# Kernel optimization log

Hardware: AMD Instinct MI355X
Metric: run time of the kernel (lower is better)

## Reference

```python
import jax, jax.numpy as jnp
import numpy as np

BATCH, L, D_OUT, D_HID = 8, 8192, 512, 256
R_MIN, R_MAX, MAX_PHASE = 0.9, 0.999, 6.28


def setup_inputs() -> dict:
    key = jax.random.key(0)
    ks = jax.random.split(key, 10)
    x = jax.random.normal(ks[0], (BATCH, L, D_OUT), jnp.float32)
    # input_dense (nn.Dense(d_out)) params
    W = jax.random.normal(ks[1], (D_OUT, D_OUT), jnp.float32) / jnp.sqrt(jnp.float32(D_OUT))
    b = jnp.zeros((D_OUT,), jnp.float32)
    # nu_log / theta_log per the flax initializers
    u1 = jax.random.uniform(ks[2], (D_HID,), jnp.float32)
    nu_log = jnp.log(-0.5 * jnp.log(u1 * (R_MAX**2 - R_MIN**2) + R_MIN**2))
    u2 = jax.random.uniform(ks[3], (D_HID,), jnp.float32)
    theta_log = jnp.log(MAX_PHASE * u2)
    diag_lambda = jnp.exp(-jnp.exp(nu_log) + 1j * jnp.exp(theta_log))
    gamma_log = jnp.log(jnp.sqrt(1.0 - jnp.abs(diag_lambda) ** 2))
    B_re = jax.random.normal(ks[4], (D_HID, D_OUT), jnp.float32) / jnp.sqrt(jnp.float32(2 * D_OUT))
    B_im = jax.random.normal(ks[5], (D_HID, D_OUT), jnp.float32) / jnp.sqrt(jnp.float32(2 * D_OUT))
    C_re = jax.random.normal(ks[6], (D_OUT, D_HID), jnp.float32) / jnp.sqrt(jnp.float32(D_HID))
    C_im = jax.random.normal(ks[7], (D_OUT, D_HID), jnp.float32) / jnp.sqrt(jnp.float32(D_HID))
    D = jax.random.normal(ks[8], (D_OUT,), jnp.float32)
    return {"x": x, "W": W, "b": b, "nu_log": nu_log, "theta_log": theta_log,
            "gamma_log": gamma_log, "B_re": B_re, "B_im": B_im,
            "C_re": C_re, "C_im": C_im, "D": D}


def _binop(q_i, q_j):
    # associative op for diagonal linear recurrence h_t = A_t h_{t-1} + b_t
    A_i, b_i = q_i
    A_j, b_j = q_j
    return (A_j * A_i, A_j * b_i + b_j)


def reference(x, W, b, nu_log, theta_log, gamma_log, B_re, B_im, C_re, C_im, D):
    xp = x @ W + b                                            # [B,L,d_out]
    lam = jnp.exp(-jnp.exp(nu_log) + 1j * jnp.exp(theta_log))  # [N] complex
    B_norm = (B_re + 1j * B_im) * jnp.exp(gamma_log)[:, None]  # [N,d_out]
    Bu = xp.astype(B_norm.dtype) @ B_norm.T                    # [B,L,N] complex
    Lam = jnp.broadcast_to(lam, Bu.shape)
    # parallel scan over sequence axis (axis=1); elementwise binop, batch broadcasts
    _, h = jax.lax.associative_scan(_binop, (Lam, Bu), axis=1)  # [B,L,N]
    C = C_re + 1j * C_im                                        # [d_out,N]
    outputs = jnp.real(h @ C.T) + D * xp                        # [B,L,d_out]
    return outputs, h[:, -1]
```

## Files before the change

kernel.cpp:

```cpp
#include <hip/hip_runtime.h>
#include <hip/hip_bf16.h>
#include <math.h>

#define BATCH   8
#define SEQL    8192
#define DOUTD   512
#define DHID    256
#define MTOT    (BATCH*SEQL)
#define CHUNKS  128
#define CHUNKLN 64
#define SQUAR   6

typedef __bf16 bh;
typedef __bf16 bh8 __attribute__((ext_vector_type(8)));
typedef __bf16 bh2 __attribute__((ext_vector_type(2)));
typedef float  f32x4 __attribute__((ext_vector_type(4)));


__global__ void setup_kernel(const float4* __restrict__ x, bh* __restrict__ xh,
                             const float* __restrict__ W, float* __restrict__ Wt,
                             const float* __restrict__ nu_log, const float* __restrict__ theta_log,
                             const float* __restrict__ gamma_log, const float* __restrict__ Bre,
                             const float* __restrict__ Bim, const float* __restrict__ bvec,
                             const float* __restrict__ Dvec,
                             float* lamRe, float* lamIm, float* lamSRe, float* lamSIm,
                             float* gamma, float* bB, float* bD) {
    int bid = blockIdx.x;
    const int tid = threadIdx.x;
    if (bid < 16384) {
        long i = (long)bid * 256 + tid;
        float4 a = x[2 * i], c = x[2 * i + 1];
        bh8 o;
        o[0] = (bh)a.x; o[1] = (bh)a.y; o[2] = (bh)a.z; o[3] = (bh)a.w;
        o[4] = (bh)c.x; o[5] = (bh)c.y; o[6] = (bh)c.z; o[7] = (bh)c.w;
        *(bh8*)(xh + i * 8) = o;
        return;
    }
    bid -= 16384;
    if (bid < 64) {
        __shared__ float t[64][65];
        const int bx = bid & 7, by = bid >> 3;
        const int r0 = by * 64, c0 = bx * 64;
        const int tr = tid >> 4;
        const int tc = (tid & 15) * 4;
#pragma unroll
        for (int rr = 0; rr < 64; rr += 16) {
            float4 v = *(const float4*)&W[(size_t)(r0 + tr + rr) * 512 + c0 + tc];
            t[tr + rr][tc + 0] = v.x; t[tr + rr][tc + 1] = v.y;
            t[tr + rr][tc + 2] = v.z; t[tr + rr][tc + 3] = v.w;
        }
        __syncthreads();
#pragma unroll
        for (int rr = 0; rr < 64; rr += 16) {
            const int orow = tr + rr;
            float4 o;
            o.x = t[tc + 0][orow]; o.y = t[tc + 1][orow];
            o.z = t[tc + 2][orow]; o.w = t[tc + 3][orow];
            *(float4*)&Wt[(size_t)(c0 + orow) * 512 + r0 + tc] = o;
        }
        return;
    }
    bid -= 64;
    if (bid == 0) {
        for (int t = tid; t < 512; t += 256) bD[t] = bvec[t] * Dvec[t];
        int t = tid;
        if (t < 256) {
            float nu = expf(nu_log[t]);
            float th = expf(theta_log[t]);
            float mag = expf(-nu);
            float lr = mag * cosf(th), li = mag * sinf(th);
            lamRe[t] = lr; lamIm[t] = li;
            float pr = lr, pi = li;
            for (int s = 0; s < SQUAR; ++s) { float nr = pr*pr - pi*pi, ni = 2.f*pr*pi; pr = nr; pi = ni; }
            lamSRe[t] = pr; lamSIm[t] = pi;
            gamma[t] = expf(gamma_log[t]);
        }
        return;
    }
    const int t = bid - 1;
    __shared__ float rr[256], ri[256];
    float b0 = bvec[tid], b1 = bvec[tid + 256];
    float pr = b0 * Bre[(size_t)t * 512 + tid] + b1 * Bre[(size_t)t * 512 + tid + 256];
    float pi = b0 * Bim[(size_t)t * 512 + tid] + b1 * Bim[(size_t)t * 512 + tid + 256];
    rr[tid] = pr; ri[tid] = pi;
    __syncthreads();
    for (int s = 128; s > 0; s >>= 1) {
        if (tid < s) { rr[tid] += rr[tid + s]; ri[tid] += ri[tid + s]; }
        __syncthreads();
    }
    if (tid == 0) {
        float g = expf(gamma_log[t]);
        bB[2 * t]     = rr[0] * g;
        bB[2 * t + 1] = ri[0] * g;
    }
}

__global__ void prepBC_kernel(const float* __restrict__ Wt, const float* __restrict__ Bre,
                              const float* __restrict__ Bim, const float* __restrict__ gamma,
                              bh* __restrict__ WBt,
                              const float* __restrict__ Cre, const float* __restrict__ Cim,
                              const float* __restrict__ Dvec, bh* __restrict__ WcT) {
    if (blockIdx.x < 128) {
        __shared__ float bsh[4][512];
        const int c0 = blockIdx.x * 4;
        const int tid = threadIdx.x;
        for (int i = tid; i < 2048; i += 256) {
            int ci = i >> 9, k = i & 511;
            int c = c0 + ci;
            float v = (c < 256) ? Bre[(size_t)c * 512 + k] : Bim[(size_t)(c - 256) * 512 + k];
            bsh[ci][k] = v * gamma[c & 255];
        }
        __syncthreads();
        const int j = tid * 2;
        float a0[4] = {}, a1[4] = {};
        for (int k = 0; k < 512; ++k) {
            float2 wv = *(const float2*)&Wt[(size_t)k * 512 + j];
#pragma unroll
            for (int ci = 0; ci < 4; ++ci) {
                float b = bsh[ci][k];
                a0[ci] += wv.x * b;
                a1[ci] += wv.y * b;
            }
        }
#pragma unroll
        for (int ci = 0; ci < 4; ++ci) {
            const int c = c0 + ci;
            const int r = (c < 256) ? 2 * c : 2 * (c - 256) + 1;
            WBt[(size_t)r * 512 + j]     = (bh)a0[ci];
            WBt[(size_t)r * 512 + j + 1] = (bh)a1[ci];
        }
        return;
    }
    int e = (blockIdx.x - 128) * 256 + threadIdx.x;
    int c = e >> 10, kp = e & 1023;
    float v;
    if (kp < 512) {
        int n = kp >> 1;
        v = (kp & 1) ? -Cim[c * 256 + n] : Cre[c * 256 + n];
    } else {
        v = Wt[(size_t)c * 512 + (kp - 512)] * Dvec[c];
    }
    WcT[e] = (bh)v;
}

#define MMAQ(mh, nh) \
  _Pragma("unroll") for (int ks = 0; ks < 2; ++ks) \
  _Pragma("unroll") for (int mi = 0; mi < 4; ++mi) \
  _Pragma("unroll") for (int ni = 0; ni < 2; ++ni) \
    acc[(mh)*4+mi][(nh)*2+ni] = __builtin_amdgcn_mfma_f32_16x16x32_bf16( \
        afr[mi*2+ks], bfr[ni*2+ks], acc[(mh)*4+mi][(nh)*2+ni], 0, 0, 0);

#define PH_MMA(mh, nh) \
  __builtin_amdgcn_s_barrier(); \
  __builtin_amdgcn_s_setprio(1); \
  MMAQ(mh, nh) \
  __builtin_amdgcn_s_setprio(0); \
  __builtin_amdgcn_s_barrier();

template<int KTOT, bool SPLIT_A, bool OUT_F32>
__global__ __launch_bounds__(512, 2)
void gemm_kernel(const bh* __restrict__ A0, const bh* __restrict__ A1,
                 const bh* __restrict__ Bw, const float* __restrict__ bias,
                 float* __restrict__ outF, bh* __restrict__ outH) {
    __shared__ alignas(16) bh lds[65536];
    const int tid = threadIdx.x;
    const int l = tid & 63, w = tid >> 6;
    const int wm = w >> 2, wn = w & 3;
    const int bid = blockIdx.x, nwg = gridDim.x;
    const int swz = (bid & 7) * (nwg >> 3) + (bid >> 3);
    const int rowBase = (swz >> 1) * 256;
    const int colBase = (swz & 1) * 256;
    const int rsub = l & 15, g = l >> 4;
    const int r7 = rsub & 7;
    const int sl0 = ((0 + g) ^ r7) * 8;
    const int sl1 = ((4 + g) ^ r7) * 8;
    const int st_r  = tid >> 3;
    const int st_sl = ((tid & 7) ^ (st_r & 7)) * 8;
    const int st_ld = (tid & 7) * 8;

    f32x4 acc[8][4] = {};
    bh8 afr[8];
    bh8 bfr[4];

    const int NT  = KTOT / 64;
    const int NIT = NT / 2;

    auto stageA = [&](int t, int half, int bufsel) {
        const int k0 = t * 64;
        const bh* As = A0; int kk = k0;
        if (SPLIT_A && k0 >= 512) { As = A1; kk = k0 - 512; }
        bh* lb = &lds[bufsel * 32768];
#pragma unroll
        for (int j = 0; j < 2; ++j) {
            const int rt = half * 128 + j * 64 + st_r;
            const bh* ga = As + (size_t)(rowBase + rt) * 512 + kk + st_sl;
            __builtin_amdgcn_global_load_lds(
                (const __attribute__((address_space(1))) void*)ga,
                (__attribute__((address_space(3))) void*)&lb[rt * 64 + st_ld], 16, 0, 0);
        }
    };
    auto stageB = [&](int t, int half, int bufsel) {
        const int k0 = t * 64;
        bh* lb = &lds[bufsel * 32768 + 16384];
#pragma unroll
        for (int j = 0; j < 2; ++j) {
            const int rt = half * 128 + j * 64 + st_r;
            const bh* gb = Bw + (size_t)(colBase + rt) * KTOT + k0 + st_sl;
            __builtin_amdgcn_global_load_lds(
                (const __attribute__((address_space(1))) void*)gb,
                (__attribute__((address_space(3))) void*)&lb[rt * 64 + st_ld], 16, 0, 0);
        }
    };
    auto dsA = [&](int mh, int bufsel) {
        const bh* lb = &lds[bufsel * 32768];
#pragma unroll
        for (int mi = 0; mi < 4; ++mi) {
            const int row = wm * 128 + (mh * 4 + mi) * 16 + rsub;
            afr[mi * 2 + 0] = *(const bh8*)&lb[row * 64 + sl0];
            afr[mi * 2 + 1] = *(const bh8*)&lb[row * 64 + sl1];
        }
    };
    auto dsB = [&](int nh, int bufsel) {
        const bh* lb = &lds[bufsel * 32768 + 16384];
#pragma unroll
        for (int ni = 0; ni < 2; ++ni) {
            const int row = wn * 64 + (nh * 2 + ni) * 16 + rsub;
            bfr[ni * 2 + 0] = *(const bh8*)&lb[row * 64 + sl0];
            bfr[ni * 2 + 1] = *(const bh8*)&lb[row * 64 + sl1];
        }
    };

    stageA(0, 0, 0); stageA(0, 1, 0); stageB(0, 0, 0); stageB(0, 1, 0);
    asm volatile("s_waitcnt vmcnt(0)" ::: "memory");
    __builtin_amdgcn_sched_barrier(0);
    __builtin_amdgcn_s_barrier();

    for (int i = 0; i < NIT; ++i) {
        const int t0 = 2 * i, t1 = 2 * i + 1;
        dsA(0, 0); dsB(0, 0);
        stageA(t1, 0, 1); stageA(t1, 1, 1);
        PH_MMA(0, 0)
        dsB(1, 0);
        stageB(t1, 0, 1); stageB(t1, 1, 1);
        PH_MMA(0, 1)
        dsA(1, 0);
        PH_MMA(1, 1)
        dsB(0, 0);
        __builtin_amdgcn_s_barrier();
        __builtin_amdgcn_s_setprio(1);
        MMAQ(1, 0)
        __builtin_amdgcn_s_setprio(0);
        asm volatile("s_waitcnt vmcnt(0)" ::: "memory");
        __builtin_amdgcn_sched_barrier(0);
        __builtin_amdgcn_s_barrier();
        dsA(0, 1); dsB(0, 1);
        if (t0 + 2 < NT) { stageA(t0 + 2, 0, 0); stageA(t0 + 2, 1, 0); }
        PH_MMA(0, 0)
        dsB(1, 1);
        if (t0 + 2 < NT) { stageB(t0 + 2, 0, 0); stageB(t0 + 2, 1, 0); }
        PH_MMA(0, 1)
        dsA(1, 1);
        PH_MMA(1, 1)
        dsB(0, 1);
        __builtin_amdgcn_s_barrier();
        __builtin_amdgcn_s_setprio(1);
        MMAQ(1, 0)
        __builtin_amdgcn_s_setprio(0);
        asm volatile("s_waitcnt vmcnt(0)" ::: "memory");
        __builtin_amdgcn_sched_barrier(0);
        __builtin_amdgcn_s_barrier();
    }

#pragma unroll
    for (int m = 0; m < 8; ++m)
#pragma unroll
        for (int j = 0; j < 4; ++j) {
            const int row = rowBase + wm * 128 + m * 16 + g * 4 + j;
#pragma unroll
            for (int n = 0; n < 4; ++n) {
                const int col = colBase + wn * 64 + n * 16 + rsub;
                float v = acc[m][n][j] + bias[col];
                if (OUT_F32) outF[(size_t)row * 512 + col] = v;
                else         outH[(size_t)row * 512 + col] = (bh)v;
            }
        }
}

__global__ void scan1_kernel(const bh* __restrict__ Bu, const float* __restrict__ lamRe,
                             const float* __restrict__ lamIm, float* __restrict__ carRe,
                             float* __restrict__ carIm) {
    int b = blockIdx.x >> 7, c = blockIdx.x & (CHUNKS - 1);
    int n = threadIdx.x;
    float lr = lamRe[n], li = lamIm[n];
    float hr = 0.f, hi = 0.f;
    const unsigned* p = (const unsigned*)Bu + ((size_t)(b * SEQL + c * CHUNKLN)) * 256 + n;
    for (int i = 0; i < CHUNKLN; ++i) {
        unsigned u = *p;
        float br = __uint_as_float(u << 16);
        float bi = __uint_as_float(u & 0xffff0000u);
        float nr = lr * hr - li * hi + br;
        float ni = lr * hi + li * hr + bi;
        hr = nr; hi = ni; p += 256;
    }
    carRe[(size_t)blockIdx.x * 256 + n] = hr;
    carIm[(size_t)blockIdx.x * 256 + n] = hi;
}

__global__ void scan2_kernel(const float* __restrict__ carRe, const float* __restrict__ carIm,
                             const float* __restrict__ lamSRe, const float* __restrict__ lamSIm,
                             float* __restrict__ iniRe, float* __restrict__ iniIm) {
    int b = blockIdx.x, n = threadIdx.x;
    float lr = lamSRe[n], li = lamSIm[n];
    float hr = 0.f, hi = 0.f;
    for (int c = 0; c < CHUNKS; ++c) {
        size_t idx = ((size_t)b * CHUNKS + c) * 256 + n;
        iniRe[idx] = hr; iniIm[idx] = hi;
        float cr = carRe[idx], ci = carIm[idx];
        float nr = lr * hr - li * hi + cr;
        float ni = lr * hi + li * hr + ci;
        hr = nr; hi = ni;
    }
}

__global__ void scan3_kernel(bh* __restrict__ Bu, const float* __restrict__ lamRe,
                             const float* __restrict__ lamIm, const float* __restrict__ iniRe,
                             const float* __restrict__ iniIm, float* __restrict__ outTail,
                             int tailN) {
    int b = blockIdx.x >> 7, c = blockIdx.x & (CHUNKS - 1);
    int n = threadIdx.x;
    float lr = lamRe[n], li = lamIm[n];
    size_t idx = (size_t)blockIdx.x * 256 + n;
    float hr = iniRe[idx], hi = iniIm[idx];
    unsigned* p = (unsigned*)Bu + ((size_t)(b * SEQL + c * CHUNKLN)) * 256 + n;
    for (int i = 0; i < CHUNKLN; ++i) {
        unsigned u = *p;
        float br = __uint_as_float(u << 16);
        float bi = __uint_as_float(u & 0xffff0000u);
        float nr = lr * hr - li * hi + br;
        float ni = lr * hi + li * hr + bi;
        hr = nr; hi = ni;
        bh2 o; o[0] = (bh)hr; o[1] = (bh)hi;
        *(bh2*)p = o;
        p += 256;
    }
    if (c == CHUNKS - 1) {
        if (tailN >= 4096) {
            outTail[b * 256 + n]        = hr;
            outTail[2048 + b * 256 + n] = hi;
        } else {
            outTail[b * 256 + n] = hr;
        }
    }
}

extern "C" void kernel_launch(void* const* d_in, const int* in_sizes, int n_in,
                              void* d_out, int out_size, void* d_ws, size_t ws_size,
                              hipStream_t stream) {
    const float* x        = (const float*)d_in[0];
    const float* W        = (const float*)d_in[1];
    const float* bvec     = (const float*)d_in[2];
    const float* nu_log   = (const float*)d_in[3];
    const float* theta_lg = (const float*)d_in[4];
    const float* gamma_lg = (const float*)d_in[5];
    const float* Bre      = (const float*)d_in[6];
    const float* Bim      = (const float*)d_in[7];
    const float* Cre      = (const float*)d_in[8];
    const float* Cim      = (const float*)d_in[9];
    const float* Dvec     = (const float*)d_in[10];

    char* ws = (char*)d_ws;
    bh* xh   = (bh*)(ws);
    bh* bu   = (bh*)(ws + 67108864);
    bh* wbt  = (bh*)(ws + 134217728);
    bh* wct  = (bh*)(ws + 134217728 + 524288);
    float* Wt = (float*)(ws + 134217728 + 524288 + 1048576);
    float* sm = (float*)(ws + 134217728 + 524288 + 1048576 + 1048576);
    float* bB = sm;
    float* bD = sm + 512;
    float* lamRe  = sm + 1024;
    float* lamIm  = sm + 1280;
    float* lamSRe = sm + 1536;
    float* lamSIm = sm + 1792;
    float* gamma  = sm + 2048;
    float* carRe  = sm + 2304;
    float* carIm  = carRe + (size_t)BATCH * CHUNKS * 256;
    float* iniRe  = carIm + (size_t)BATCH * CHUNKS * 256;
    float* iniIm  = iniRe + (size_t)BATCH * CHUNKS * 256;

    float* outF    = (float*)d_out;
    float* outTail = outF + (size_t)MTOT * DOUTD;
    int tailN = out_size - MTOT * DOUTD;

    setup_kernel<<<16705, 256, 0, stream>>>((const float4*)x, xh, W, Wt,
                                            nu_log, theta_lg, gamma_lg, Bre, Bim, bvec, Dvec,
                                            lamRe, lamIm, lamSRe, lamSIm, gamma, bB, bD);
    prepBC_kernel<<<2176, 256, 0, stream>>>(Wt, Bre, Bim, gamma, wbt, Cre, Cim, Dvec, wct);

    gemm_kernel<512, false, false><<<512, 512, 0, stream>>>(xh, nullptr, wbt, bB, nullptr, bu);

    scan1_kernel<<<BATCH * CHUNKS, 256, 0, stream>>>(bu, lamRe, lamIm, carRe, carIm);
    scan2_kernel<<<BATCH, 256, 0, stream>>>(carRe, carIm, lamSRe, lamSIm, iniRe, iniIm);
    scan3_kernel<<<BATCH * CHUNKS, 256, 0, stream>>>(bu, lamRe, lamIm, iniRe, iniIm, outTail, tailN);

    gemm_kernel<1024, true, true><<<512, 512, 0, stream>>>(bu, xh, wct, bD, outF, nullptr);
}
```

Measured before the change: 246.0 us.

## Deepen GEMM prefetch with per-quadrant LDS staging and partial vmcnt waits

Reorganizes the LDS layout so each A/B half-tile is stored contiguously per warp quadrant. Global-to-LDS loads are issued at quadrant granularity, as soon as the quadrant's previous contents are consumed. The loop now waits with vmcnt(6) instead of draining all loads, so more loads stay in flight across barriers and global latency overlaps the MFMA phases. This relies on exact counting of outstanding loads and on the buffer-reuse ordering being correct. A miscount would create a race on LDS contents.

```diff
diff --git a/kernel.cpp b/kernel.cpp
--- a/kernel.cpp
+++ b/kernel.cpp
@@ -159,7 +159,7 @@
 
 template<int KTOT, bool SPLIT_A, bool OUT_F32>
 __global__ __launch_bounds__(512, 2)
-void gemm_kernel(const bh* __restrict__ A0, const bh* __restrict__ A1,
+void gemm_kernel(const bh* __restrict__ A0v, const bh* __restrict__ A1v,
                  const bh* __restrict__ Bw, const float* __restrict__ bias,
                  float* __restrict__ outF, bh* __restrict__ outH) {
     __shared__ alignas(16) bh lds[65536];
@@ -174,9 +174,8 @@
     const int r7 = rsub & 7;
     const int sl0 = ((0 + g) ^ r7) * 8;
     const int sl1 = ((4 + g) ^ r7) * 8;
-    const int st_r  = tid >> 3;
-    const int st_sl = ((tid & 7) ^ (st_r & 7)) * 8;
-    const int st_ld = (tid & 7) * 8;
+    const int strl = tid >> 3;
+    const int stsl = ((tid & 7) ^ (strl & 7)) * 8;
 
     f32x4 acc[8][4] = {};
     bh8 afr[8];
@@ -185,88 +184,98 @@
     const int NT  = KTOT / 64;
     const int NIT = NT / 2;
 
-    auto stageA = [&](int t, int half, int bufsel) {
+    auto stageA = [&](int t, int mh, int bufsel) {
         const int k0 = t * 64;
-        const bh* As = A0; int kk = k0;
-        if (SPLIT_A && k0 >= 512) { As = A1; kk = k0 - 512; }
-        bh* lb = &lds[bufsel * 32768];
+        const bh* As = A0v; int kk = k0;
+        if (SPLIT_A && k0 >= 512) { As = A1v; kk = k0 - 512; }
+        bh* lb = &lds[bufsel * 32768 + mh * 8192];
 #pragma unroll
         for (int j = 0; j < 2; ++j) {
-            const int rt = half * 128 + j * 64 + st_r;
-            const bh* ga = As + (size_t)(rowBase + rt) * 512 + kk + st_sl;
+            const int gr = j * 128 + mh * 64 + strl;
+            const bh* ga = As + (size_t)(rowBase + gr) * 512 + kk + stsl;
             __builtin_amdgcn_global_load_lds(
                 (const __attribute__((address_space(1))) void*)ga,
-                (__attribute__((address_space(3))) void*)&lb[rt * 64 + st_ld], 16, 0, 0);
+                (__attribute__((address_space(3))) void*)&lb[j * 4096 + tid * 8], 16, 0, 0);
         }
     };
-    auto stageB = [&](int t, int half, int bufsel) {
+    auto stageB = [&](int t, int nh, int bufsel) {
         const int k0 = t * 64;
-        bh* lb = &lds[bufsel * 32768 + 16384];
+        bh* lb = &lds[bufsel * 32768 + 16384 + nh * 8192];
 #pragma unroll
         for (int j = 0; j < 2; ++j) {
-            const int rt = half * 128 + j * 64 + st_r;
-            const bh* gb = Bw + (size_t)(colBase + rt) * KTOT + k0 + st_sl;
+            const int wnj = j * 2 + (strl >> 5);
+            const int gr = wnj * 64 + nh * 32 + (strl & 31);
+            const bh* gb = Bw + (size_t)(colBase + gr) * KTOT + k0 + stsl;
             __builtin_amdgcn_global_load_lds(
                 (const __attribute__((address_space(1))) void*)gb,
-                (__attribute__((address_space(3))) void*)&lb[rt * 64 + st_ld], 16, 0, 0);
+                (__attribute__((address_space(3))) void*)&lb[j * 4096 + tid * 8], 16, 0, 0);
         }
     };
     auto dsA = [&](int mh, int bufsel) {
-        const bh* lb = &lds[bufsel * 32768];
+        const bh* lb = &lds[bufsel * 32768 + mh * 8192 + wm * 4096];
 #pragma unroll
         for (int mi = 0; mi < 4; ++mi) {
-            const int row = wm * 128 + (mh * 4 + mi) * 16 + rsub;
-            afr[mi * 2 + 0] = *(const bh8*)&lb[row * 64 + sl0];
-            afr[mi * 2 + 1] = *(const bh8*)&lb[row * 64 + sl1];
+            const int ro = (mi * 16 + rsub) * 64;
+            afr[mi * 2 + 0] = *(const bh8*)&lb[ro + sl0];
+            afr[mi * 2 + 1] = *(const bh8*)&lb[ro + sl1];
         }
     };
     auto dsB = [&](int nh, int bufsel) {
-        const bh* lb = &lds[bufsel * 32768 + 16384];
+        const bh* lb = &lds[bufsel * 32768 + 16384 + nh * 8192 + wn * 2048];
 #pragma unroll
         for (int ni = 0; ni < 2; ++ni) {
-            const int row = wn * 64 + (nh * 2 + ni) * 16 + rsub;
-            bfr[ni * 2 + 0] = *(const bh8*)&lb[row * 64 + sl0];
-            bfr[ni * 2 + 1] = *(const bh8*)&lb[row * 64 + sl1];
+            const int ro = (ni * 16 + rsub) * 64;
+            bfr[ni * 2 + 0] = *(const bh8*)&lb[ro + sl0];
+            bfr[ni * 2 + 1] = *(const bh8*)&lb[ro + sl1];
         }
     };
 
-    stageA(0, 0, 0); stageA(0, 1, 0); stageB(0, 0, 0); stageB(0, 1, 0);
-    asm volatile("s_waitcnt vmcnt(0)" ::: "memory");
+    stageA(0, 0, 0); stageB(0, 0, 0); stageB(0, 1, 0); stageA(0, 1, 0);
+    stageA(1, 0, 1); stageB(1, 1, 1); stageA(1, 1, 1);
+    asm volatile("s_waitcnt vmcnt(6)" ::: "memory");
     __builtin_amdgcn_sched_barrier(0);
     __builtin_amdgcn_s_barrier();
 
     for (int i = 0; i < NIT; ++i) {
         const int t0 = 2 * i, t1 = 2 * i + 1;
+        const bool p2 = (t0 + 2 < NT);
+        const bool p3 = (t1 + 2 < NT);
         dsA(0, 0); dsB(0, 0);
-        stageA(t1, 0, 1); stageA(t1, 1, 1);
+        stageB(t1, 0, 1);
         PH_MMA(0, 0)
         dsB(1, 0);
-        stageB(t1, 0, 1); stageB(t1, 1, 1);
+        if (p2) stageA(t0 + 2, 0, 0);
         PH_MMA(0, 1)
         dsA(1, 0);
+        if (p2) stageB(t0 + 2, 1, 0);
         PH_MMA(1, 1)
         dsB(0, 0);
+        if (p2) stageA(t0 + 2, 1, 0);
         __builtin_amdgcn_s_barrier();
         __builtin_amdgcn_s_setprio(1);
         MMAQ(1, 0)
         __builtin_amdgcn_s_setprio(0);
-        asm volatile("s_waitcnt vmcnt(0)" ::: "memory");
+        if (p2) { asm volatile("s_waitcnt vmcnt(6)" ::: "memory"); }
+        else    { asm volatile("s_waitcnt vmcnt(0)" ::: "memory"); }
         __builtin_amdgcn_sched_barrier(0);
         __builtin_amdgcn_s_barrier();
         dsA(0, 1); dsB(0, 1);
-        if (t0 + 2 < NT) { stageA(t0 + 2, 0, 0); stageA(t0 + 2, 1, 0); }
+        if (p2) stageB(t0 + 2, 0, 0);
         PH_MMA(0, 0)
         dsB(1, 1);
-        if (t0 + 2 < NT) { stageB(t0 + 2, 0, 0); stageB(t0 + 2, 1, 0); }
+        if (p3) stageA(t1 + 2, 0, 1);
         PH_MMA(0, 1)
         dsA(1, 1);
+        if (p3) stageB(t1 + 2, 1, 1);
         PH_MMA(1, 1)
         dsB(0, 1);
+        if (p3) stageA(t1 + 2, 1, 1);
         __builtin_amdgcn_s_barrier();
         __builtin_amdgcn_s_setprio(1);
         MMAQ(1, 0)
         __builtin_amdgcn_s_setprio(0);
-        asm volatile("s_waitcnt vmcnt(0)" ::: "memory");
+        if (p3) { asm volatile("s_waitcnt vmcnt(6)" ::: "memory"); }
+        else    { asm volatile("s_waitcnt vmcnt(0)" ::: "memory"); }
         __builtin_amdgcn_sched_barrier(0);
         __builtin_amdgcn_s_barrier();
     }
```

Result: faster. 238.4 us (-3.1%).
